# Kernel tuning notes

Hardware: AMD Instinct MI355X
Metric: run time of the kernel (lower is better)

The kernel has to match this reference:

```python
import jax, jax.numpy as jnp
import numpy as np

D_MODEL = 384; N_LAYER = 8; N_MELS = 80; D_STATE = 16; EXPAND = 2; D_CONV = 4
D_INNER = EXPAND * D_MODEL           # 768
DT_RANK = (D_MODEL + 15) // 16       # 24 ('auto')
B = 4; L = 512


def setup_inputs() -> dict:
    key = jax.random.key(0)
    ks = jax.random.split(key, 12)
    g = lambda k, shape, s=0.02: jax.random.normal(k, shape, dtype=jnp.float32) * s
    A_log = jnp.tile(jnp.log(jnp.arange(1, D_STATE + 1, dtype=jnp.float32))[None, None, :],
                     (N_LAYER, D_INNER, 1))
    return {
        "x": jax.random.normal(ks[0], (B, L, N_MELS), dtype=jnp.float32),
        "enc_output": jax.random.normal(ks[1], (B, L, D_MODEL), dtype=jnp.float32),
        "w_in": g(ks[2], (N_MELS, D_MODEL)),
        "b_in": jnp.zeros((D_MODEL,), jnp.float32),
        "ln_w": jnp.ones((N_LAYER, D_MODEL), jnp.float32),
        "inproj_w": g(ks[3], (N_LAYER, D_MODEL, 2 * D_INNER)),
        "conv_w": g(ks[4], (N_LAYER, D_INNER, D_CONV), 0.1),
        "conv_b": jnp.zeros((N_LAYER, D_INNER), jnp.float32),
        "xproj_w": g(ks[5], (N_LAYER, D_INNER, DT_RANK + 2 * D_STATE)),
        "dtproj_w": g(ks[6], (N_LAYER, DT_RANK, D_INNER), 0.1),
        "dtproj_b": g(ks[7], (N_LAYER, D_INNER), 0.1),
        "A_log": A_log,
        "D": jnp.ones((N_LAYER, D_INNER), jnp.float32),
        "outproj_w": g(ks[8], (N_LAYER, D_INNER, D_MODEL)),
        "normf_w": jnp.ones((D_MODEL,), jnp.float32),
        "w_out": g(ks[9], (D_MODEL, N_MELS)),
    }


def rmsnorm(x, w, eps=1e-5):
    return x * jax.lax.rsqrt(jnp.mean(x * x, axis=-1, keepdims=True) + eps) * w


def selective_scan(u, delta, A, Bm, Cm, Dp):
    # u, delta: (b,l,d); A: (d,n); Bm, Cm: (b,l,n); Dp: (d,)
    dA = jnp.exp(jnp.einsum('bld,dn->bldn', delta, A))          # (b,l,d,n)
    dBu = jnp.einsum('bld,bln,bld->bldn', delta, Bm, u)          # (b,l,d,n)

    def step(h, xs):
        dA_t, dBu_t, C_t = xs                                    # (b,d,n),(b,d,n),(b,n)
        h = dA_t * h + dBu_t
        y = jnp.einsum('bdn,bn->bd', h, C_t)
        return h, y

    h0 = jnp.zeros((u.shape[0], u.shape[2], A.shape[1]), u.dtype)
    _, ys = jax.lax.scan(step, h0, (dA.transpose(1, 0, 2, 3),
                                    dBu.transpose(1, 0, 2, 3),
                                    Cm.transpose(1, 0, 2)))
    return ys.transpose(1, 0, 2) + u * Dp                        # (b,l,d)


def mamba_layer(x, ln, ip, cw, cb, xp, dw, db, al, dp, op):
    h = rmsnorm(x, ln)
    xr = h @ ip                                                  # (b,l,2*d_inner)
    xs, res = jnp.split(xr, 2, axis=-1)
    # depthwise causal conv1d: pad d_conv-1 on the left, truncate to L
    xc = jax.lax.conv_general_dilated(xs.transpose(0, 2, 1), cw[:, None, :],
                                      (1,), [(D_CONV - 1, 0)],
                                      feature_group_count=D_INNER)
    xs = jax.nn.silu((xc + cb[None, :, None]).transpose(0, 2, 1))
    xdbl = xs @ xp                                               # (b,l,dt_rank+2n)
    dt = xdbl[..., :DT_RANK]
    Bm = xdbl[..., DT_RANK:DT_RANK + D_STATE]
    Cm = xdbl[..., DT_RANK + D_STATE:]
    delta = jax.nn.softplus(dt @ dw + db)
    y = selective_scan(xs, delta, -jnp.exp(al), Bm, Cm, dp)
    y = y * jax.nn.silu(res)
    return x + y @ op


def reference(x, enc_output, w_in, b_in, ln_w, inproj_w, conv_w, conv_b,
              xproj_w, dtproj_w, dtproj_b, A_log, D, outproj_w, normf_w, w_out):
    h = x @ w_in + b_in
    half = N_LAYER // 2
    for i in range(half):
        h = mamba_layer(h, ln_w[i], inproj_w[i], conv_w[i], conv_b[i], xproj_w[i],
                        dtproj_w[i], dtproj_b[i], A_log[i], D[i], outproj_w[i])
    # soft attention: decoder states attend over encoder output
    scores = jnp.einsum('bqd,bkd->bqk', h, enc_output)
    h = jnp.einsum('bqk,bkd->bqd', jax.nn.softmax(scores, axis=-1), enc_output)
    for i in range(half, N_LAYER):
        h = mamba_layer(h, ln_w[i], inproj_w[i], conv_w[i], conv_b[i], xproj_w[i],
                        dtproj_w[i], dtproj_b[i], A_log[i], D[i], outproj_w[i])
    h = rmsnorm(h, normf_w)
    return h @ w_out
```

## Files before the change

kernel.cpp:

```cpp
#include <hip/hip_runtime.h>
#include <hip/hip_bf16.h>
#include <math.h>

#define D_MODEL 384
#define N_LAYER 8
#define N_MELS  80
#define D_STATE 16
#define D_CONV  4
#define D_INNER 768
#define DT_RANK 24
#define BB      4
#define LL      512
#define MTOK    (BB*LL)

#define BMt 64
#define BNt 64
#define BKt 16

#define XP_N   56
#define XPS    12
#define XPKC   64

typedef __attribute__((ext_vector_type(8))) short bf16x8;
typedef __attribute__((ext_vector_type(4))) short bf16x4;
typedef __attribute__((ext_vector_type(4))) float f32x4;

__device__ __forceinline__ float silu_f(float x) { return x / (1.f + __expf(-x)); }
__device__ __forceinline__ short bf_raw(float x) {
  __hip_bfloat16 h = __float2bfloat16(x);
  return *reinterpret_cast<short*>(&h);
}

template<int EPI>
__global__ __launch_bounds__(256) void gemm_f32(
    const float* __restrict__ A, int lda,
    const float* __restrict__ W, int ldw,
    const float* __restrict__ bias,
    float* __restrict__ C, int ldc,
    int M, int N, int K)
{
  __shared__ float As[BKt][BMt];
  __shared__ float Ws[BKt][BNt];
  const int tid = threadIdx.x;
  const int tx = tid & 15, ty = tid >> 4;
  const int m0 = blockIdx.y * BMt, n0 = blockIdx.x * BNt;
  const int am = tid >> 2, ak4 = (tid & 3) << 2;
  const int wk = tid >> 4, wn4 = (tid & 15) << 2;

  float acc[4][4] = {};

  for (int k0 = 0; k0 < K; k0 += BKt) {
    float4 va = make_float4(0.f, 0.f, 0.f, 0.f);
    {
      int m = m0 + am;
      if (m < M) {
        if (k0 + ak4 + 3 < K) {
          va = *reinterpret_cast<const float4*>(&A[(size_t)m * lda + k0 + ak4]);
        } else {
          float t[4];
          #pragma unroll
          for (int j = 0; j < 4; ++j)
            t[j] = (k0 + ak4 + j < K) ? A[(size_t)m * lda + k0 + ak4 + j] : 0.f;
          va = make_float4(t[0], t[1], t[2], t[3]);
        }
      }
    }
    As[ak4 + 0][am] = va.x;
    As[ak4 + 1][am] = va.y;
    As[ak4 + 2][am] = va.z;
    As[ak4 + 3][am] = va.w;

    float4 vw = make_float4(0.f, 0.f, 0.f, 0.f);
    {
      int kw = k0 + wk;
      if (kw < K) {
        if (n0 + wn4 + 3 < N) {
          vw = *reinterpret_cast<const float4*>(&W[(size_t)kw * ldw + n0 + wn4]);
        } else {
          float t[4];
          #pragma unroll
          for (int j = 0; j < 4; ++j)
            t[j] = (n0 + wn4 + j < N) ? W[(size_t)kw * ldw + n0 + wn4 + j] : 0.f;
          vw = make_float4(t[0], t[1], t[2], t[3]);
        }
      }
    }
    *reinterpret_cast<float4*>(&Ws[wk][wn4]) = vw;

    __syncthreads();
    #pragma unroll
    for (int kk = 0; kk < BKt; ++kk) {
      const float4 a4 = *reinterpret_cast<const float4*>(&As[kk][ty << 2]);
      const float4 w4 = *reinterpret_cast<const float4*>(&Ws[kk][tx << 2]);
      float av[4] = {a4.x, a4.y, a4.z, a4.w};
      float wv[4] = {w4.x, w4.y, w4.z, w4.w};
      #pragma unroll
      for (int i = 0; i < 4; ++i)
        #pragma unroll
        for (int j = 0; j < 4; ++j)
          acc[i][j] += av[i] * wv[j];
    }
    __syncthreads();
  }

  #pragma unroll
  for (int i = 0; i < 4; ++i) {
    int row = m0 + (ty << 2) + i;
    if (row >= M) continue;
    #pragma unroll
    for (int j = 0; j < 4; ++j) {
      int col = n0 + (tx << 2) + j;
      if (col >= N) continue;
      float v = acc[i][j];
      if (EPI == 1) v += bias[col];
      C[(size_t)row * ldc + col] = v;
    }
  }
}

template<int EPI>
__global__ __launch_bounds__(256) void gemm_bf16(
    const __hip_bfloat16* __restrict__ A,
    const __hip_bfloat16* __restrict__ WT,
    const float* __restrict__ resid,
    float* __restrict__ C, int ldc,
    int M, int N, int K)
{
  __shared__ __align__(16) __hip_bfloat16 Asl[64][72];
  __shared__ __align__(16) __hip_bfloat16 Bsl[64][72];
  const int tid = threadIdx.x;
  const int wave = tid >> 6, lane = tid & 63;
  const int m0 = blockIdx.y * 64, n0 = blockIdx.x * 64;
  const int lrow = tid >> 2;
  const int lk   = (tid & 3) << 4;
  const int g16 = lane >> 4;
  const int l16 = lane & 15;

  f32x4 acc[4] = {};

  for (int k0 = 0; k0 < K; k0 += 64) {
    const uint4* ga = reinterpret_cast<const uint4*>(&A[(size_t)(m0 + lrow) * K + k0 + lk]);
    uint4* la = reinterpret_cast<uint4*>(&Asl[lrow][lk]);
    la[0] = ga[0]; la[1] = ga[1];
    const uint4* gb = reinterpret_cast<const uint4*>(&WT[(size_t)(n0 + lrow) * K + k0 + lk]);
    uint4* lb = reinterpret_cast<uint4*>(&Bsl[lrow][lk]);
    lb[0] = gb[0]; lb[1] = gb[1];
    __syncthreads();
    #pragma unroll
    for (int kk = 0; kk < 64; kk += 32) {
      bf16x8 a = *reinterpret_cast<const bf16x8*>(&Asl[wave * 16 + l16][kk + g16 * 8]);
      #pragma unroll
      for (int f = 0; f < 4; ++f) {
        bf16x8 b = *reinterpret_cast<const bf16x8*>(&Bsl[f * 16 + l16][kk + g16 * 8]);
        acc[f] = __builtin_amdgcn_mfma_f32_16x16x32_bf16(a, b, acc[f], 0, 0, 0);
      }
    }
    __syncthreads();
  }

  #pragma unroll
  for (int f = 0; f < 4; ++f) {
    #pragma unroll
    for (int r = 0; r < 4; ++r) {
      int row = m0 + wave * 16 + g16 * 4 + r;
      int col = n0 + f * 16 + l16;
      float v = acc[f][r];
      if (EPI == 3) v += resid[(size_t)row * ldc + col];
      C[(size_t)row * ldc + col] = v;
    }
  }
}

__global__ __launch_bounds__(256) void gemm_bf16_bat(
    const __hip_bfloat16* __restrict__ A, size_t sA,
    const __hip_bfloat16* __restrict__ WT, size_t sW,
    float* __restrict__ C, size_t sC,
    int M, int N, int K)
{
  A  += (size_t)blockIdx.z * sA;
  WT += (size_t)blockIdx.z * sW;
  C  += (size_t)blockIdx.z * sC;
  __shared__ __align__(16) __hip_bfloat16 Asl[64][72];
  __shared__ __align__(16) __hip_bfloat16 Bsl[64][72];
  const int tid = threadIdx.x;
  const int wave = tid >> 6, lane = tid & 63;
  const int m0 = blockIdx.y * 64, n0 = blockIdx.x * 64;
  const int lrow = tid >> 2;
  const int lk   = (tid & 3) << 4;
  const int g16 = lane >> 4;
  const int l16 = lane & 15;

  f32x4 acc[4] = {};

  for (int k0 = 0; k0 < K; k0 += 64) {
    const uint4* ga = reinterpret_cast<const uint4*>(&A[(size_t)(m0 + lrow) * K + k0 + lk]);
    uint4* la = reinterpret_cast<uint4*>(&Asl[lrow][lk]);
    la[0] = ga[0]; la[1] = ga[1];
    const uint4* gb = reinterpret_cast<const uint4*>(&WT[(size_t)(n0 + lrow) * K + k0 + lk]);
    uint4* lb = reinterpret_cast<uint4*>(&Bsl[lrow][lk]);
    lb[0] = gb[0]; lb[1] = gb[1];
    __syncthreads();
    #pragma unroll
    for (int kk = 0; kk < 64; kk += 32) {
      bf16x8 a = *reinterpret_cast<const bf16x8*>(&Asl[wave * 16 + l16][kk + g16 * 8]);
      #pragma unroll
      for (int f = 0; f < 4; ++f) {
        bf16x8 b = *reinterpret_cast<const bf16x8*>(&Bsl[f * 16 + l16][kk + g16 * 8]);
        acc[f] = __builtin_amdgcn_mfma_f32_16x16x32_bf16(a, b, acc[f], 0, 0, 0);
      }
    }
    __syncthreads();
  }

  #pragma unroll
  for (int f = 0; f < 4; ++f) {
    #pragma unroll
    for (int r = 0; r < 4; ++r) {
      int row = m0 + wave * 16 + g16 * 4 + r;
      int col = n0 + f * 16 + l16;
      C[(size_t)row * N + col] = acc[f][r];
    }
  }
}

__global__ __launch_bounds__(256) void xproj_splitk_bf16(
    const __hip_bfloat16* __restrict__ A,
    const __hip_bfloat16* __restrict__ WT,
    float* __restrict__ part)
{
  __shared__ __align__(16) __hip_bfloat16 Asl[64][72];
  __shared__ __align__(16) __hip_bfloat16 Bsl[64][72];
  const int tid = threadIdx.x;
  const int wave = tid >> 6, lane = tid & 63;
  const int split = blockIdx.x;
  const int m0 = blockIdx.y * 64;
  const int kbase = split * XPKC;
  const int lrow = tid >> 2;
  const int lk   = (tid & 3) << 4;
  const int g16 = lane >> 4;
  const int l16 = lane & 15;

  f32x4 acc[4] = {};

  const uint4* ga = reinterpret_cast<const uint4*>(&A[(size_t)(m0 + lrow) * D_INNER + kbase + lk]);
  uint4* la = reinterpret_cast<uint4*>(&Asl[lrow][lk]);
  la[0] = ga[0]; la[1] = ga[1];
  const uint4* gb = reinterpret_cast<const uint4*>(&WT[(size_t)lrow * D_INNER + kbase + lk]);
  uint4* lb = reinterpret_cast<uint4*>(&Bsl[lrow][lk]);
  lb[0] = gb[0]; lb[1] = gb[1];
  __syncthreads();
  #pragma unroll
  for (int kk = 0; kk < 64; kk += 32) {
    bf16x8 a = *reinterpret_cast<const bf16x8*>(&Asl[wave * 16 + l16][kk + g16 * 8]);
    #pragma unroll
    for (int f = 0; f < 4; ++f) {
      bf16x8 b = *reinterpret_cast<const bf16x8*>(&Bsl[f * 16 + l16][kk + g16 * 8]);
      acc[f] = __builtin_amdgcn_mfma_f32_16x16x32_bf16(a, b, acc[f], 0, 0, 0);
    }
  }

  #pragma unroll
  for (int f = 0; f < 4; ++f) {
    #pragma unroll
    for (int r = 0; r < 4; ++r) {
      int row = m0 + wave * 16 + g16 * 4 + r;
      int col = f * 16 + l16;
      part[((size_t)split * MTOK + row) * 64 + col] = acc[f][r];
    }
  }
}

__global__ __launch_bounds__(256) void xproj_reduce_kernel(
    const float* __restrict__ part, float* __restrict__ xdbl)
{
  int idx = blockIdx.x * 256 + threadIdx.x;
  if (idx >= MTOK * XP_N) return;
  int m = idx / XP_N, col = idx - m * XP_N;
  float s = 0.f;
  #pragma unroll
  for (int p = 0; p < XPS; ++p)
    s += part[((size_t)p * MTOK + m) * 64 + col];
  xdbl[idx] = s;
}

__global__ __launch_bounds__(256) void wconv_t_kernel(
    const float* __restrict__ src, __hip_bfloat16* __restrict__ dst,
    int K, int N, size_t ldl)
{
  __shared__ float tile[32][33];
  int l = blockIdx.z;
  int kb = blockIdx.y * 32, nb = blockIdx.x * 32;
  int tn = threadIdx.x & 31, tk = threadIdx.x >> 5;
  const float* s = src + (size_t)l * K * N;
  __hip_bfloat16* dd = dst + (size_t)l * ldl;
  #pragma unroll
  for (int i = 0; i < 4; ++i) {
    int k = kb + tk + i * 8, n = nb + tn;
    tile[tk + i * 8][tn] = (k < K && n < N) ? s[(size_t)k * N + n] : 0.f;
  }
  __syncthreads();
  #pragma unroll
  for (int i = 0; i < 4; ++i) {
    int n = nb + tk + i * 8, k = kb + tn;
    if (n < N && k < K) dd[(size_t)n * K + k] = __float2bfloat16(tile[tn][tk + i * 8]);
  }
}

__global__ __launch_bounds__(256) void f2b_kernel(
    const float* __restrict__ src, __hip_bfloat16* __restrict__ dst, int n)
{
  int i = (blockIdx.x * 256 + threadIdx.x) * 4;
  if (i >= n) return;
  float4 v = *reinterpret_cast<const float4*>(&src[i]);
  bf16x4 o;
  o[0] = bf_raw(v.x); o[1] = bf_raw(v.y); o[2] = bf_raw(v.z); o[3] = bf_raw(v.w);
  *reinterpret_cast<bf16x4*>(&dst[i]) = o;
}

__global__ __launch_bounds__(256) void softmax_rows_kernel(
    const float* __restrict__ scores, __hip_bfloat16* __restrict__ P)
{
  int row = (blockIdx.x * 256 + threadIdx.x) >> 6;
  int lane = threadIdx.x & 63;
  if (row >= BB * LL) return;
  const float* s = scores + (size_t)row * LL + lane * 8;
  float4 v0 = *reinterpret_cast<const float4*>(s);
  float4 v1 = *reinterpret_cast<const float4*>(s + 4);
  float mx = fmaxf(fmaxf(fmaxf(v0.x, v0.y), fmaxf(v0.z, v0.w)),
                   fmaxf(fmaxf(v1.x, v1.y), fmaxf(v1.z, v1.w)));
  #pragma unroll
  for (int off = 32; off; off >>= 1) mx = fmaxf(mx, __shfl_xor(mx, off, 64));
  float e[8];
  e[0] = __expf(v0.x - mx); e[1] = __expf(v0.y - mx);
  e[2] = __expf(v0.z - mx); e[3] = __expf(v0.w - mx);
  e[4] = __expf(v1.x - mx); e[5] = __expf(v1.y - mx);
  e[6] = __expf(v1.z - mx); e[7] = __expf(v1.w - mx);
  float sum = ((e[0] + e[1]) + (e[2] + e[3])) + ((e[4] + e[5]) + (e[6] + e[7]));
  #pragma unroll
  for (int off = 32; off; off >>= 1) sum += __shfl_xor(sum, off, 64);
  float inv = 1.f / sum;
  bf16x8 o;
  #pragma unroll
  for (int j = 0; j < 8; ++j) o[j] = bf_raw(e[j] * inv);
  *reinterpret_cast<bf16x8*>(&P[(size_t)row * LL + lane * 8]) = o;
}

__global__ __launch_bounds__(256) void rmsnorm_kernel(
    const float* __restrict__ x, const float* __restrict__ w,
    float* __restrict__ out, __hip_bfloat16* __restrict__ outb, int M, int N)
{
  int gw = (blockIdx.x * blockDim.x + threadIdx.x) >> 6;
  int lane = threadIdx.x & 63;
  if (gw >= M) return;
  const float* row = x + (size_t)gw * N;
  float ss = 0.f;
  for (int j = lane; j < N; j += 64) { float v = row[j]; ss += v * v; }
  #pragma unroll
  for (int off = 32; off; off >>= 1) ss += __shfl_xor(ss, off, 64);
  float scale = rsqrtf(ss / (float)N + 1e-5f);
  float* orow = out ? out + (size_t)gw * N : nullptr;
  __hip_bfloat16* brow = outb + (size_t)gw * N;
  for (int j = lane; j < N; j += 64) {
    float v = row[j] * scale * w[j];
    if (orow) orow[j] = v;
    brow[j] = __float2bfloat16(v);
  }
}

__global__ __launch_bounds__(256) void conv_silu_kernel(
    const float* __restrict__ xr, const float* __restrict__ cw,
    const float* __restrict__ cb, __hip_bfloat16* __restrict__ xsb)
{
  int idx = blockIdx.x * 256 + threadIdx.x;
  if (idx >= MTOK * D_INNER) return;
  int m = idx / D_INNER;
  int d = idx - m * D_INNER;
  int b = m >> 9, l = m & 511;
  float acc = 0.f;
  #pragma unroll
  for (int k = 0; k < D_CONV; ++k) {
    int t = l - (D_CONV - 1) + k;
    if (t >= 0) acc += xr[((size_t)(b * LL + t)) * (2 * D_INNER) + d] * cw[d * D_CONV + k];
  }
  acc += cb[d];
  xsb[idx] = __float2bfloat16(silu_f(acc));
}

#define SC3_T  16
#define SC3_NC 32
__global__ __launch_bounds__(512) void scan_kernel5(
    const __hip_bfloat16* __restrict__ xsb,
    const float* __restrict__ xdbl,
    const float* __restrict__ A_log,
    const float* __restrict__ Dp,
    const float* __restrict__ dtw,
    const float* __restrict__ dtb,
    const float* __restrict__ xr,
    __hip_bfloat16* __restrict__ yg)
{
  __shared__ float sdelta[LL];
  __shared__ float su[LL];
  __shared__ float sdw[DT_RANK];
  __shared__ float sP[SC3_NC][D_STATE + 1];
  __shared__ float sS[SC3_NC][D_STATE + 1];
  __shared__ float sH0[SC3_NC][D_STATE + 1];
  __shared__ float sY[LL][5];

  const int id = blockIdx.x;
  const int r  = id / 96;
  const int G  = id % 96;
  const int b  = G / 24;
  const int d  = (G % 24) * 32 + r;

  const int tid = threadIdx.x;
  const int n = tid & 15;
  const int c = tid >> 4;

  if (tid < DT_RANK) sdw[tid] = dtw[tid * D_INNER + d];
  __syncthreads();

  {
    const int l = tid;
    const size_t m = (size_t)(b * LL + l);
    float acc = dtb[d];
    const float* xrow = &xdbl[m * 56];
    #pragma unroll
    for (int k4 = 0; k4 < DT_RANK; k4 += 4) {
      float4 xv = *reinterpret_cast<const float4*>(&xrow[k4]);
      acc += xv.x * sdw[k4] + xv.y * sdw[k4 + 1] + xv.z * sdw[k4 + 2] + xv.w * sdw[k4 + 3];
    }
    sdelta[l] = (acc > 20.f) ? acc : log1pf(__expf(acc));
    su[l]     = __bfloat162float(xsb[m * D_INNER + d]);
  }

  const float Aval = -__expf(A_log[d * D_STATE + n]);
  const int l0 = c * SC3_T;
  const size_t mbase = (size_t)(b * LL + l0);

  float Bv_s[SC3_T];
  #pragma unroll
  for (int t = 0; t < SC3_T; ++t)
    Bv_s[t] = xdbl[(mbase + t) * 56 + DT_RANK + n];

  __syncthreads();

  float a_s[SC3_T], dbu_s[SC3_T];
  {
    float P = 1.f, S = 0.f;
    #pragma unroll
    for (int t = 0; t < SC3_T; ++t) {
      int l = l0 + t;
      float dv = sdelta[l];
      float uv = su[l];
      float a = __expf(dv * Aval);
      float dbu = (dv * Bv_s[t]) * uv;
      P *= a;
      S = a * S + dbu;
      a_s[t] = a;
      dbu_s[t] = dbu;
    }
    sP[c][n] = P;
    sS[c][n] = S;
  }

  float Cv_s[SC3_T];
  #pragma unroll
  for (int t = 0; t < SC3_T; ++t)
    Cv_s[t] = xdbl[(mbase + t) * 56 + DT_RANK + D_STATE + n];

  __syncthreads();

  {
    const int c2 = tid & 31;
    const int n2 = tid >> 5;
    float p = sP[c2][n2];
    float s = sS[c2][n2];
    #pragma unroll
    for (int k = 1; k <= 16; k <<= 1) {
      float pp = __shfl_up(p, k, 64);
      float sp = __shfl_up(s, k, 64);
      if (c2 >= k) { s = p * sp + s; p = p * pp; }
    }
    if (c2 == 0) sH0[0][n2] = 0.f;
    if (c2 < 31) sH0[c2 + 1][n2] = s;
  }
  __syncthreads();

  {
    float h = sH0[c][n];
    #pragma unroll
    for (int t = 0; t < SC3_T; ++t) {
      int l = l0 + t;
      h = a_s[t] * h + dbu_s[t];
      float contrib = h * Cv_s[t];
      contrib += __shfl_xor(contrib, 1, 64);
      contrib += __shfl_xor(contrib, 2, 64);
      if ((n & 3) == 0) sY[l][n >> 2] = contrib;
    }
  }
  __syncthreads();

  {
    const int l = tid;
    const size_t m = (size_t)(b * LL + l);
    float y = (sY[l][0] + sY[l][1]) + (sY[l][2] + sY[l][3]) + su[l] * Dp[d];
    float rres = xr[m * (2 * D_INNER) + D_INNER + d];
    yg[m * D_INNER + d] = __float2bfloat16(y * silu_f(rres));
  }
}

extern "C" void kernel_launch(void* const* d_in, const int* in_sizes, int n_in,
                              void* d_out, int out_size, void* d_ws, size_t ws_size,
                              hipStream_t stream) {
  const float* x        = (const float*)d_in[0];
  const float* enc      = (const float*)d_in[1];
  const float* w_in     = (const float*)d_in[2];
  const float* b_in     = (const float*)d_in[3];
  const float* ln_w     = (const float*)d_in[4];
  const float* inproj_w = (const float*)d_in[5];
  const float* conv_w   = (const float*)d_in[6];
  const float* conv_b   = (const float*)d_in[7];
  const float* xproj_w  = (const float*)d_in[8];
  const float* dtproj_w = (const float*)d_in[9];
  const float* dtproj_b = (const float*)d_in[10];
  const float* A_log    = (const float*)d_in[11];
  const float* Dvec     = (const float*)d_in[12];
  const float* outproj_w= (const float*)d_in[13];
  const float* normf_w  = (const float*)d_in[14];
  const float* w_out    = (const float*)d_in[15];

  float* ws = (float*)d_ws;
  float* h     = ws; ws += MTOK * D_MODEL;
  float* hn    = ws; ws += MTOK * D_MODEL;
  float* xr    = ws; ws += MTOK * 2 * D_INNER;
  float* xdbl  = ws; ws += MTOK * XP_N;
  float* xpart = ws; ws += XPS * MTOK * 64;
  float* h2    = ws; ws += MTOK * D_MODEL;
  float* scores= ws; ws += BB * LL * LL;
  __hip_bfloat16* hn_bf = (__hip_bfloat16*)ws; ws += MTOK * D_MODEL / 2;
  __hip_bfloat16* xs_bf = (__hip_bfloat16*)ws; ws += MTOK * D_INNER / 2;
  __hip_bfloat16* yg_bf = (__hip_bfloat16*)ws; ws += MTOK * D_INNER / 2;
  __hip_bfloat16* h_bf  = (__hip_bfloat16*)ws; ws += MTOK * D_MODEL / 2;
  __hip_bfloat16* P_bf  = (__hip_bfloat16*)ws; ws += BB * LL * LL / 2;
  __hip_bfloat16* enc_bf= (__hip_bfloat16*)ws; ws += BB * LL * D_MODEL / 2;
  __hip_bfloat16* encT  = (__hip_bfloat16*)ws; ws += BB * LL * D_MODEL / 2;
  __hip_bfloat16* WinT  = (__hip_bfloat16*)ws; ws += N_LAYER * D_MODEL * 2 * D_INNER / 2;
  __hip_bfloat16* WoutT = (__hip_bfloat16*)ws; ws += N_LAYER * D_INNER * D_MODEL / 2;
  __hip_bfloat16* XpT   = (__hip_bfloat16*)ws; ws += N_LAYER * 64 * D_INNER / 2;

  dim3 blk256(256), blk512(512);

  wconv_t_kernel<<<dim3(2 * D_INNER / 32, D_MODEL / 32, N_LAYER), blk256, 0, stream>>>(
      inproj_w, WinT, D_MODEL, 2 * D_INNER, (size_t)2 * D_INNER * D_MODEL);
  wconv_t_kernel<<<dim3(D_MODEL / 32, D_INNER / 32, N_LAYER), blk256, 0, stream>>>(
      outproj_w, WoutT, D_INNER, D_MODEL, (size_t)D_MODEL * D_INNER);
  wconv_t_kernel<<<dim3((XP_N + 31) / 32, D_INNER / 32, N_LAYER), blk256, 0, stream>>>(
      xproj_w, XpT, D_INNER, XP_N, (size_t)64 * D_INNER);
  f2b_kernel<<<(BB * LL * D_MODEL / 4 + 255) / 256, blk256, 0, stream>>>(
      enc, enc_bf, BB * LL * D_MODEL);
  wconv_t_kernel<<<dim3(D_MODEL / 32, LL / 32, BB), blk256, 0, stream>>>(
      enc, encT, LL, D_MODEL, (size_t)D_MODEL * LL);

  gemm_f32<1><<<dim3(D_MODEL / BNt, MTOK / BMt), blk256, 0, stream>>>(
      x, N_MELS, w_in, D_MODEL, b_in, h, D_MODEL, MTOK, D_MODEL, N_MELS);

  auto mamba = [&](float* hcur, int i) {
    rmsnorm_kernel<<<MTOK * 64 / 256, blk256, 0, stream>>>(
        hcur, ln_w + (size_t)i * D_MODEL, nullptr, hn_bf, MTOK, D_MODEL);
    gemm_bf16<0><<<dim3(2 * D_INNER / 64, MTOK / 64), blk256, 0, stream>>>(
        hn_bf, WinT + (size_t)i * D_MODEL * 2 * D_INNER, nullptr,
        xr, 2 * D_INNER, MTOK, 2 * D_INNER, D_MODEL);
    conv_silu_kernel<<<MTOK * D_INNER / 256, blk256, 0, stream>>>(
        xr, conv_w + (size_t)i * D_INNER * D_CONV, conv_b + (size_t)i * D_INNER, xs_bf);
    xproj_splitk_bf16<<<dim3(XPS, MTOK / 64), blk256, 0, stream>>>(
        xs_bf, XpT + (size_t)i * 64 * D_INNER, xpart);
    xproj_reduce_kernel<<<(MTOK * XP_N + 255) / 256, blk256, 0, stream>>>(xpart, xdbl);
    scan_kernel5<<<BB * D_INNER, blk512, 0, stream>>>(
        xs_bf, xdbl, A_log + (size_t)i * D_INNER * D_STATE, Dvec + (size_t)i * D_INNER,
        dtproj_w + (size_t)i * DT_RANK * D_INNER, dtproj_b + (size_t)i * D_INNER,
        xr, yg_bf);
    gemm_bf16<3><<<dim3(D_MODEL / 64, MTOK / 64), blk256, 0, stream>>>(
        yg_bf, WoutT + (size_t)i * D_INNER * D_MODEL, hcur,
        hcur, D_MODEL, MTOK, D_MODEL, D_INNER);
  };

  for (int i = 0; i < N_LAYER / 2; ++i) mamba(h, i);

  f2b_kernel<<<(MTOK * D_MODEL / 4 + 255) / 256, blk256, 0, stream>>>(
      h, h_bf, MTOK * D_MODEL);
  gemm_bf16_bat<<<dim3(LL / 64, LL / 64, BB), blk256, 0, stream>>>(
      h_bf, (size_t)LL * D_MODEL, enc_bf, (size_t)LL * D_MODEL,
      scores, (size_t)LL * LL, LL, LL, D_MODEL);
  softmax_rows_kernel<<<(BB * LL * 64) / 256, blk256, 0, stream>>>(scores, P_bf);
  gemm_bf16_bat<<<dim3(D_MODEL / 64, LL / 64, BB), blk256, 0, stream>>>(
      P_bf, (size_t)LL * LL, encT, (size_t)D_MODEL * LL,
      h2, (size_t)LL * D_MODEL, LL, D_MODEL, LL);

  for (int i = N_LAYER / 2; i < N_LAYER; ++i) mamba(h2, i);

  rmsnorm_kernel<<<MTOK * 64 / 256, blk256, 0, stream>>>(h2, normf_w, hn, hn_bf, MTOK, D_MODEL);
  gemm_f32<0><<<dim3((N_MELS + BNt - 1) / BNt, MTOK / BMt), blk256, 0, stream>>>(
      hn, D_MODEL, w_out, N_MELS, nullptr, (float*)d_out, N_MELS, MTOK, N_MELS, D_MODEL);
}
```

Measured before the change: 849.6 us.

## Store in-projection output in bf16 and scan two channels per block

The in-projection GEMM now writes its output as bf16 instead of fp32, which halves the traffic for the xr tensor read by conv_silu and by the scan's gating step. The scan kernel now handles two adjacent inner channels per block, using packed 32-bit loads and stores for u, the residual gate and the output, and launches half as many blocks. The two channels share the B/C loads from xdbl and reuse dBu recomputation instead of keeping it in registers. The cost is some precision loss on the pre-conv activations and gate, plus higher register and LDS use per block.

```diff
diff --git a/kernel.cpp b/kernel.cpp
--- a/kernel.cpp
+++ b/kernel.cpp
@@ -29,6 +29,10 @@
 __device__ __forceinline__ short bf_raw(float x) {
   __hip_bfloat16 h = __float2bfloat16(x);
   return *reinterpret_cast<short*>(&h);
+}
+__device__ __forceinline__ float bfu(unsigned short u) {
+  unsigned v = ((unsigned)u) << 16;
+  return *reinterpret_cast<float*>(&v);
 }
 
 template<int EPI>
@@ -118,13 +122,14 @@
   }
 }
 
-template<int EPI>
+template<int EPI, int OBF>
 __global__ __launch_bounds__(256) void gemm_bf16(
     const __hip_bfloat16* __restrict__ A,
     const __hip_bfloat16* __restrict__ WT,
     const float* __restrict__ resid,
-    float* __restrict__ C, int ldc,
-    int M, int N, int K)
+    float* __restrict__ C,
+    __hip_bfloat16* __restrict__ Cb,
+    int ldc, int M, int N, int K)
 {
   __shared__ __align__(16) __hip_bfloat16 Asl[64][72];
   __shared__ __align__(16) __hip_bfloat16 Bsl[64][72];
@@ -166,7 +171,8 @@
       int col = n0 + f * 16 + l16;
       float v = acc[f][r];
       if (EPI == 3) v += resid[(size_t)row * ldc + col];
-      C[(size_t)row * ldc + col] = v;
+      if (OBF) Cb[(size_t)row * ldc + col] = __float2bfloat16(v);
+      else     C[(size_t)row * ldc + col] = v;
     }
   }
 }
@@ -368,7 +374,7 @@
 }
 
 __global__ __launch_bounds__(256) void conv_silu_kernel(
-    const float* __restrict__ xr, const float* __restrict__ cw,
+    const __hip_bfloat16* __restrict__ xrb, const float* __restrict__ cw,
     const float* __restrict__ cb, __hip_bfloat16* __restrict__ xsb)
 {
   int idx = blockIdx.x * 256 + threadIdx.x;
@@ -380,92 +386,102 @@
   #pragma unroll
   for (int k = 0; k < D_CONV; ++k) {
     int t = l - (D_CONV - 1) + k;
-    if (t >= 0) acc += xr[((size_t)(b * LL + t)) * (2 * D_INNER) + d] * cw[d * D_CONV + k];
+    if (t >= 0)
+      acc += __bfloat162float(xrb[((size_t)(b * LL + t)) * (2 * D_INNER) + d]) * cw[d * D_CONV + k];
   }
   acc += cb[d];
   xsb[idx] = __float2bfloat16(silu_f(acc));
 }
 
-#define SC3_T  16
-#define SC3_NC 32
-__global__ __launch_bounds__(512) void scan_kernel5(
+#define SC6_T  16
+#define SC6_NC 32
+__global__ __launch_bounds__(512) void scan_kernel6(
     const __hip_bfloat16* __restrict__ xsb,
     const float* __restrict__ xdbl,
     const float* __restrict__ A_log,
     const float* __restrict__ Dp,
     const float* __restrict__ dtw,
     const float* __restrict__ dtb,
-    const float* __restrict__ xr,
+    const __hip_bfloat16* __restrict__ xrb,
     __hip_bfloat16* __restrict__ yg)
 {
-  __shared__ float sdelta[LL];
-  __shared__ float su[LL];
-  __shared__ float sdw[DT_RANK];
-  __shared__ float sP[SC3_NC][D_STATE + 1];
-  __shared__ float sS[SC3_NC][D_STATE + 1];
-  __shared__ float sH0[SC3_NC][D_STATE + 1];
-  __shared__ float sY[LL][5];
+  __shared__ float sdelta[2][LL];
+  __shared__ float su[2][LL];
+  __shared__ float sdw[2][DT_RANK];
+  __shared__ float sP[2][SC6_NC][D_STATE + 1];
+  __shared__ float sS[2][SC6_NC][D_STATE + 1];
+  __shared__ float sH0[2][SC6_NC][D_STATE + 1];
+  __shared__ float sY[2][LL][5];
 
   const int id = blockIdx.x;
-  const int r  = id / 96;
-  const int G  = id % 96;
-  const int b  = G / 24;
-  const int d  = (G % 24) * 32 + r;
+  const int r  = id / 48;
+  const int G  = id % 48;
+  const int b  = G / 12;
+  const int q  = G % 12;
+  const int d0 = q * 64 + 2 * r;
+  const int d1 = d0 + 1;
 
   const int tid = threadIdx.x;
   const int n = tid & 15;
   const int c = tid >> 4;
 
-  if (tid < DT_RANK) sdw[tid] = dtw[tid * D_INNER + d];
+  if (tid < DT_RANK) {
+    sdw[0][tid] = dtw[tid * D_INNER + d0];
+    sdw[1][tid] = dtw[tid * D_INNER + d1];
+  }
   __syncthreads();
 
   {
     const int l = tid;
     const size_t m = (size_t)(b * LL + l);
-    float acc = dtb[d];
+    float acc0 = dtb[d0], acc1 = dtb[d1];
     const float* xrow = &xdbl[m * 56];
     #pragma unroll
     for (int k4 = 0; k4 < DT_RANK; k4 += 4) {
       float4 xv = *reinterpret_cast<const float4*>(&xrow[k4]);
-      acc += xv.x * sdw[k4] + xv.y * sdw[k4 + 1] + xv.z * sdw[k4 + 2] + xv.w * sdw[k4 + 3];
-    }
-    sdelta[l] = (acc > 20.f) ? acc : log1pf(__expf(acc));
-    su[l]     = __bfloat162float(xsb[m * D_INNER + d]);
-  }
-
-  const float Aval = -__expf(A_log[d * D_STATE + n]);
-  const int l0 = c * SC3_T;
+      acc0 += xv.x * sdw[0][k4] + xv.y * sdw[0][k4 + 1] + xv.z * sdw[0][k4 + 2] + xv.w * sdw[0][k4 + 3];
+      acc1 += xv.x * sdw[1][k4] + xv.y * sdw[1][k4 + 1] + xv.z * sdw[1][k4 + 2] + xv.w * sdw[1][k4 + 3];
+    }
+    sdelta[0][l] = (acc0 > 20.f) ? acc0 : log1pf(__expf(acc0));
+    sdelta[1][l] = (acc1 > 20.f) ? acc1 : log1pf(__expf(acc1));
+    unsigned uu = *reinterpret_cast<const unsigned*>(&xsb[m * D_INNER + d0]);
+    su[0][l] = bfu((unsigned short)(uu & 0xffff));
+    su[1][l] = bfu((unsigned short)(uu >> 16));
+  }
+
+  const float Aval0 = -__expf(A_log[d0 * D_STATE + n]);
+  const float Aval1 = -__expf(A_log[d1 * D_STATE + n]);
+  const int l0 = c * SC6_T;
   const size_t mbase = (size_t)(b * LL + l0);
 
-  float Bv_s[SC3_T];
-  #pragma unroll
-  for (int t = 0; t < SC3_T; ++t)
+  float Bv_s[SC6_T];
+  #pragma unroll
+  for (int t = 0; t < SC6_T; ++t)
     Bv_s[t] = xdbl[(mbase + t) * 56 + DT_RANK + n];
 
   __syncthreads();
 
-  float a_s[SC3_T], dbu_s[SC3_T];
+  float a_s[2][SC6_T];
   {
-    float P = 1.f, S = 0.f;
-    #pragma unroll
-    for (int t = 0; t < SC3_T; ++t) {
+    float P0 = 1.f, S0 = 0.f, P1 = 1.f, S1 = 0.f;
+    #pragma unroll
+    for (int t = 0; t < SC6_T; ++t) {
       int l = l0 + t;
-      float dv = sdelta[l];
-      float uv = su[l];
-      float a = __expf(dv * Aval);
-      float dbu = (dv * Bv_s[t]) * uv;
-      P *= a;
-      S = a * S + dbu;
-      a_s[t] = a;
-      dbu_s[t] = dbu;
-    }
-    sP[c][n] = P;
-    sS[c][n] = S;
-  }
-
-  float Cv_s[SC3_T];
-  #pragma unroll
-  for (int t = 0; t < SC3_T; ++t)
+      float dv0 = sdelta[0][l], uv0 = su[0][l];
+      float dv1 = sdelta[1][l], uv1 = su[1][l];
+      float a0 = __expf(dv0 * Aval0);
+      float a1 = __expf(dv1 * Aval1);
+      P0 *= a0; S0 = a0 * S0 + (dv0 * Bv_s[t]) * uv0;
+      P1 *= a1; S1 = a1 * S1 + (dv1 * Bv_s[t]) * uv1;
+      a_s[0][t] = a0; a_s[1][t] = a1;
+    }
+    sP[0][c][n] = P0; sS[0][c][n] = S0;
+    sP[1][c][n] = P1; sS[1][c][n] = S1;
+  }
+
+  float Cv_s[SC6_T];
+  #pragma unroll
+  for (int t = 0; t < SC6_T; ++t)
     Cv_s[t] = xdbl[(mbase + t) * 56 + DT_RANK + D_STATE + n];
 
   __syncthreads();
@@ -473,29 +489,37 @@
   {
     const int c2 = tid & 31;
     const int n2 = tid >> 5;
-    float p = sP[c2][n2];
-    float s = sS[c2][n2];
-    #pragma unroll
-    for (int k = 1; k <= 16; k <<= 1) {
-      float pp = __shfl_up(p, k, 64);
-      float sp = __shfl_up(s, k, 64);
-      if (c2 >= k) { s = p * sp + s; p = p * pp; }
-    }
-    if (c2 == 0) sH0[0][n2] = 0.f;
-    if (c2 < 31) sH0[c2 + 1][n2] = s;
+    #pragma unroll
+    for (int dd = 0; dd < 2; ++dd) {
+      float p = sP[dd][c2][n2];
+      float s = sS[dd][c2][n2];
+      #pragma unroll
+      for (int k = 1; k <= 16; k <<= 1) {
+        float pp = __shfl_up(p, k, 64);
+        float sp = __shfl_up(s, k, 64);
+        if (c2 >= k) { s = p * sp + s; p = p * pp; }
+      }
+      if (c2 == 0) sH0[dd][0][n2] = 0.f;
+      if (c2 < 31) sH0[dd][c2 + 1][n2] = s;
+    }
   }
   __syncthreads();
 
   {
-    float h = sH0[c][n];
-    #pragma unroll
-    for (int t = 0; t < SC3_T; ++t) {
+    float h0 = sH0[0][c][n];
+    float h1 = sH0[1][c][n];
+    #pragma unroll
+    for (int t = 0; t < SC6_T; ++t) {
       int l = l0 + t;
-      h = a_s[t] * h + dbu_s[t];
-      float contrib = h * Cv_s[t];
-      contrib += __shfl_xor(contrib, 1, 64);
-      contrib += __shfl_xor(contrib, 2, 64);
-      if ((n & 3) == 0) sY[l][n >> 2] = contrib;
+      float dv0 = sdelta[0][l], uv0 = su[0][l];
+      float dv1 = sdelta[1][l], uv1 = su[1][l];
+      h0 = a_s[0][t] * h0 + (dv0 * Bv_s[t]) * uv0;
+      h1 = a_s[1][t] * h1 + (dv1 * Bv_s[t]) * uv1;
+      float c0 = h0 * Cv_s[t];
+      float c1 = h1 * Cv_s[t];
+      c0 += __shfl_xor(c0, 1, 64); c0 += __shfl_xor(c0, 2, 64);
+      c1 += __shfl_xor(c1, 1, 64); c1 += __shfl_xor(c1, 2, 64);
+      if ((n & 3) == 0) { sY[0][l][n >> 2] = c0; sY[1][l][n >> 2] = c1; }
     }
   }
   __syncthreads();
@@ -503,9 +527,16 @@
   {
     const int l = tid;
     const size_t m = (size_t)(b * LL + l);
-    float y = (sY[l][0] + sY[l][1]) + (sY[l][2] + sY[l][3]) + su[l] * Dp[d];
-    float rres = xr[m * (2 * D_INNER) + D_INNER + d];
-    yg[m * D_INNER + d] = __float2bfloat16(y * silu_f(rres));
+    float y0 = (sY[0][l][0] + sY[0][l][1]) + (sY[0][l][2] + sY[0][l][3]) + su[0][l] * Dp[d0];
+    float y1 = (sY[1][l][0] + sY[1][l][1]) + (sY[1][l][2] + sY[1][l][3]) + su[1][l] * Dp[d1];
+    unsigned rr = *reinterpret_cast<const unsigned*>(&xrb[m * (2 * D_INNER) + D_INNER + d0]);
+    float r0 = bfu((unsigned short)(rr & 0xffff));
+    float r1 = bfu((unsigned short)(rr >> 16));
+    y0 *= silu_f(r0);
+    y1 *= silu_f(r1);
+    unsigned outw = ((unsigned)(unsigned short)bf_raw(y0)) |
+                    (((unsigned)(unsigned short)bf_raw(y1)) << 16);
+    *reinterpret_cast<unsigned*>(&yg[m * D_INNER + d0]) = outw;
   }
 }
 
@@ -532,11 +563,11 @@
   float* ws = (float*)d_ws;
   float* h     = ws; ws += MTOK * D_MODEL;
   float* hn    = ws; ws += MTOK * D_MODEL;
-  float* xr    = ws; ws += MTOK * 2 * D_INNER;
   float* xdbl  = ws; ws += MTOK * XP_N;
   float* xpart = ws; ws += XPS * MTOK * 64;
   float* h2    = ws; ws += MTOK * D_MODEL;
   float* scores= ws; ws += BB * LL * LL;
+  __hip_bfloat16* xr_bf = (__hip_bfloat16*)ws; ws += MTOK * 2 * D_INNER / 2;
   __hip_bfloat16* hn_bf = (__hip_bfloat16*)ws; ws += MTOK * D_MODEL / 2;
   __hip_bfloat16* xs_bf = (__hip_bfloat16*)ws; ws += MTOK * D_INNER / 2;
   __hip_bfloat16* yg_bf = (__hip_bfloat16*)ws; ws += MTOK * D_INNER / 2;
@@ -567,21 +598,21 @@
   auto mamba = [&](float* hcur, int i) {
     rmsnorm_kernel<<<MTOK * 64 / 256, blk256, 0, stream>>>(
         hcur, ln_w + (size_t)i * D_MODEL, nullptr, hn_bf, MTOK, D_MODEL);
-    gemm_bf16<0><<<dim3(2 * D_INNER / 64, MTOK / 64), blk256, 0, stream>>>(
+    gemm_bf16<0, 1><<<dim3(2 * D_INNER / 64, MTOK / 64), blk256, 0, stream>>>(
         hn_bf, WinT + (size_t)i * D_MODEL * 2 * D_INNER, nullptr,
-        xr, 2 * D_INNER, MTOK, 2 * D_INNER, D_MODEL);
+        nullptr, xr_bf, 2 * D_INNER, MTOK, 2 * D_INNER, D_MODEL);
     conv_silu_kernel<<<MTOK * D_INNER / 256, blk256, 0, stream>>>(
-        xr, conv_w + (size_t)i * D_INNER * D_CONV, conv_b + (size_t)i * D_INNER, xs_bf);
+        xr_bf, conv_w + (size_t)i * D_INNER * D_CONV, conv_b + (size_t)i * D_INNER, xs_bf);
     xproj_splitk_bf16<<<dim3(XPS, MTOK / 64), blk256, 0, stream>>>(
         xs_bf, XpT + (size_t)i * 64 * D_INNER, xpart);
     xproj_reduce_kernel<<<(MTOK * XP_N + 255) / 256, blk256, 0, stream>>>(xpart, xdbl);
-    scan_kernel5<<<BB * D_INNER, blk512, 0, stream>>>(
+    scan_kernel6<<<BB * D_INNER / 2, blk512, 0, stream>>>(
         xs_bf, xdbl, A_log + (size_t)i * D_INNER * D_STATE, Dvec + (size_t)i * D_INNER,
         dtproj_w + (size_t)i * DT_RANK * D_INNER, dtproj_b + (size_t)i * D_INNER,
-        xr, yg_bf);
-    gemm_bf16<3><<<dim3(D_MODEL / 64, MTOK / 64), blk256, 0, stream>>>(
+        xr_bf, yg_bf);
+    gemm_bf16<3, 0><<<dim3(D_MODEL / 64, MTOK / 64), blk256, 0, stream>>>(
         yg_bf, WoutT + (size_t)i * D_INNER * D_MODEL, hcur,
-        hcur, D_MODEL, MTOK, D_MODEL, D_INNER);
+        hcur, nullptr, D_MODEL, MTOK, D_MODEL, D_INNER);
   };
 
   for (int i = 0; i < N_LAYER / 2; ++i) mamba(h, i);
```

Result: faster. 735.0 us (-13.5%).
